# Kernel optimization log

Measured on AMD Instinct MI355X. Metric: run time of the kernel, lower is better.

Reference implementation:

```python
import jax, jax.numpy as jnp
import numpy as np
from jax import lax

B, K, Z, C, H, W = 32, 7, 64, 3, 64, 64
G = H + 6  # decoder grid for 'small' variant
ITERS = 3
SCALE = Z ** -0.5
EPS = 1e-8


def _pe(h, w):
    # matches SlotAttention.create_positional_embedding: shape [w, h, 4]
    ww = jnp.linspace(0.0, 1.0, w)
    hh = jnp.linspace(0.0, 1.0, h)
    a = jnp.broadcast_to((1.0 - ww)[:, None], (w, h))  # dist_right
    b = jnp.broadcast_to(ww[:, None], (w, h))          # dist_left
    c = jnp.broadcast_to(hh[None, :], (w, h))          # dist_top
    d = jnp.broadcast_to((1.0 - hh)[None, :], (w, h))  # dist_bottom
    return jnp.stack([a, b, c, d], -1)


def _ln(x, g, b):
    m = x.mean(-1, keepdims=True)
    v = ((x - m) ** 2).mean(-1, keepdims=True)
    return (x - m) * lax.rsqrt(v + 1e-5) * g + b


def _conv(x, w, b, p):
    y = lax.conv_general_dilated(x, w, (1, 1), [(p, p), (p, p)],
                                 dimension_numbers=('NCHW', 'OIHW', 'NCHW'))
    return y + b[None, :, None, None]


def setup_inputs() -> dict:
    key = jax.random.key(0)
    ks = iter(jax.random.split(key, 64))
    nrm = lambda shape, s=0.05: jax.random.normal(next(ks), shape, jnp.float32) * s
    d = {}
    d['inputs'] = jax.random.normal(next(ks), (B, C, H, W), jnp.float32)
    d['noise'] = jax.random.normal(next(ks), (B * K, Z), jnp.float32)
    d['enc_pos_w'] = nrm((4, 64)); d['enc_pos_b'] = jnp.zeros(64, jnp.float32)
    d['ec1_w'] = nrm((64, 3, 5, 5)); d['ec1_b'] = jnp.zeros(64, jnp.float32)
    d['ec2_w'] = nrm((64, 64, 5, 5)); d['ec2_b'] = jnp.zeros(64, jnp.float32)
    d['ec3_w'] = nrm((64, 64, 5, 5)); d['ec3_b'] = jnp.zeros(64, jnp.float32)
    d['ec4_w'] = nrm((64, 64, 5, 5)); d['ec4_b'] = jnp.zeros(64, jnp.float32)
    d['ln1_g'] = jnp.ones(64, jnp.float32); d['ln1_b'] = jnp.zeros(64, jnp.float32)
    d['fc1_w'] = nrm((64, 64)); d['fc1_b'] = jnp.zeros(64, jnp.float32)
    d['fc2_w'] = nrm((64, 64)); d['fc2_b'] = jnp.zeros(64, jnp.float32)
    d['lns_g'] = jnp.ones(Z, jnp.float32); d['lns_b'] = jnp.zeros(Z, jnp.float32)
    d['lnf_g'] = jnp.ones(Z, jnp.float32); d['lnf_b'] = jnp.zeros(Z, jnp.float32)
    d['q_w'] = nrm((Z, Z)); d['k_w'] = nrm((64, Z)); d['v_w'] = nrm((64, Z))
    d['mlp1_w'] = nrm((Z, 128)); d['mlp1_b'] = jnp.zeros(128, jnp.float32)
    d['mlp2_w'] = nrm((128, Z)); d['mlp2_b'] = jnp.zeros(Z, jnp.float32)
    d['gru_wih'] = nrm((3 * Z, Z)); d['gru_whh'] = nrm((3 * Z, Z))
    d['gru_bih'] = jnp.zeros(3 * Z, jnp.float32); d['gru_bhh'] = jnp.zeros(3 * Z, jnp.float32)
    d['init_slots'] = jnp.concatenate([jnp.zeros((1, Z), jnp.float32), jnp.ones((1, Z), jnp.float32)], 1)
    d['dec_pos_w'] = nrm((4, Z)); d['dec_pos_b'] = jnp.zeros(Z, jnp.float32)
    d['dc1_w'] = nrm((32, Z, 5, 5)); d['dc1_b'] = jnp.zeros(32, jnp.float32)
    d['dc2_w'] = nrm((32, 32, 5, 5)); d['dc2_b'] = jnp.zeros(32, jnp.float32)
    d['dc3_w'] = nrm((32, 32, 5, 5)); d['dc3_b'] = jnp.zeros(32, jnp.float32)
    d['dc4_w'] = nrm((4, 32, 3, 3)); d['dc4_b'] = jnp.zeros(4, jnp.float32)
    return d


def _forward(inputs, noise, enc_pos_w, enc_pos_b, ec1_w, ec1_b, ec2_w, ec2_b,
             ec3_w, ec3_b, ec4_w, ec4_b, ln1_g, ln1_b, fc1_w, fc1_b, fc2_w, fc2_b,
             lns_g, lns_b, lnf_g, lnf_b, q_w, k_w, v_w, mlp1_w, mlp1_b, mlp2_w,
             mlp2_b, gru_wih, gru_whh, gru_bih, gru_bhh, init_slots, dec_pos_w,
             dec_pos_b, dc1_w, dc1_b, dc2_w, dc2_b, dc3_w, dc3_b, dc4_w, dc4_b):
    # ---- encoder ----
    h = jax.nn.relu(_conv(inputs, ec1_w, ec1_b, 2))
    h = jax.nn.relu(_conv(h, ec2_w, ec2_b, 2))
    h = jax.nn.relu(_conv(h, ec3_w, ec3_b, 2))
    h = jax.nn.relu(_conv(h, ec4_w, ec4_b, 2))
    h = h.transpose(0, 2, 3, 1)                        # [B,H,W,64]
    pe = _pe(H, W) @ enc_pos_w + enc_pos_b             # [W,H,64] (H==W)
    h = h + pe[None]
    feat = h.reshape(B, H * W, 64)
    feat = _ln(feat, ln1_g, ln1_b)
    feat = jax.nn.relu(feat @ fc1_w + fc1_b) @ fc2_w + fc2_b
    k = feat @ k_w                                     # [B,N,Z]
    v = feat @ v_w
    # ---- slot init: Normal(loc, softplus(sp)).rsample() ----
    loc, sp = jnp.split(init_slots, 2, axis=1)
    slots = (loc + jax.nn.softplus(sp) * noise).reshape(B, K, Z)
    # ---- iterative slot attention ----
    for _ in range(ITERS):
        prev = slots
        q = (_ln(prev, lns_g, lns_b) @ q_w) * SCALE
        dots = jnp.einsum('bid,bjd->bij', q, k)        # [B,K,N]
        attn = jax.nn.softmax(dots, axis=1) + EPS      # normalize over slots
        attn = attn / attn.sum(-1, keepdims=True)      # renormalize over keys
        updates = jnp.einsum('bjd,bij->bid', v, attn)  # [B,K,Z]
        # GRU cell (single step), torch gate order r,z,n
        gi = updates.reshape(-1, Z) @ gru_wih.T + gru_bih
        gh = prev.reshape(-1, Z) @ gru_whh.T + gru_bhh
        ir, iz, inn = jnp.split(gi, 3, -1)
        hr, hz, hn = jnp.split(gh, 3, -1)
        r = jax.nn.sigmoid(ir + hr)
        zg = jax.nn.sigmoid(iz + hz)
        n = jnp.tanh(inn + r * hn)
        slots = ((1.0 - zg) * n + zg * prev.reshape(-1, Z)).reshape(B, K, Z)
        slots = slots + (jax.nn.relu(_ln(slots, lnf_g, lnf_b) @ mlp1_w + mlp1_b) @ mlp2_w + mlp2_b)
    # ---- spatial-broadcast decoder ('small') ----
    flat = slots.reshape(B * K, Z)
    zb = jnp.broadcast_to(flat[:, :, None, None], (B * K, Z, G, G))
    pe_d = (_pe(G, G) @ dec_pos_w + dec_pos_b).transpose(2, 0, 1)  # [Z,G,G]
    zb = zb + pe_d[None]
    o = jax.nn.relu(_conv(zb, dc1_w, dc1_b, 1))        # 70->68
    o = jax.nn.relu(_conv(o, dc2_w, dc2_b, 1))         # 68->66
    o = jax.nn.relu(_conv(o, dc3_w, dc3_b, 1))         # 66->64
    o = _conv(o, dc4_w, dc4_b, 1)                      # 64->64, 4ch
    x_loc = jax.nn.sigmoid(o[:, :3]).reshape(B, K, C, H, W)
    mask_logits = o[:, 3].reshape(B, K, 1, H, W)
    mask_logp = jax.nn.log_softmax(mask_logits, axis=1)
    x_orig = (inputs + 1.0) / 2.0
    recon = (x_loc * jnp.exp(mask_logp)).sum(1)
    mse = ((x_orig - recon) ** 2).sum() / B
    return mse, x_loc, mask_logp, slots


def reference(inputs, noise, enc_pos_w, enc_pos_b, ec1_w, ec1_b, ec2_w, ec2_b,
              ec3_w, ec3_b, ec4_w, ec4_b, ln1_g, ln1_b, fc1_w, fc1_b, fc2_w, fc2_b,
              lns_g, lns_b, lnf_g, lnf_b, q_w, k_w, v_w, mlp1_w, mlp1_b, mlp2_w,
              mlp2_b, gru_wih, gru_whh, gru_bih, gru_bhh, init_slots, dec_pos_w,
              dec_pos_b, dc1_w, dc1_b, dc2_w, dc2_b, dc3_w, dc3_b, dc4_w, dc4_b):
    return _forward(inputs, noise, enc_pos_w, enc_pos_b, ec1_w, ec1_b, ec2_w, ec2_b,
                    ec3_w, ec3_b, ec4_w, ec4_b, ln1_g, ln1_b, fc1_w, fc1_b, fc2_w, fc2_b,
                    lns_g, lns_b, lnf_g, lnf_b, q_w, k_w, v_w, mlp1_w, mlp1_b, mlp2_w,
                    mlp2_b, gru_wih, gru_whh, gru_bih, gru_bhh, init_slots, dec_pos_w,
                    dec_pos_b, dc1_w, dc1_b, dc2_w, dc2_b, dc3_w, dc3_b, dc4_w, dc4_b)
```

## Files before the change

kernel.cpp:

```cpp
#include <hip/hip_runtime.h>
#include <math.h>

typedef short bf16x8 __attribute__((ext_vector_type(8)));
typedef float f32x4 __attribute__((ext_vector_type(4)));

#define WS_B0   0u
#define WS_B1   4194304u
#define WS_K    8388608u
#define WS_V    16777216u
#define WS_ATTN 25165824u
#define WS_PART 26083328u
#define WS_SLOT 26327040u
#define WS_ROW  26341376u
#define SCALE_ 0.125f

#define OFF_PEB   0u
#define OFF_WCLS  160000u
#define OFF_S     180000u
#define OFF_ZB    250000u

__device__ __forceinline__ float wave_sum(float v) {
#pragma unroll
    for (int m = 32; m >= 1; m >>= 1) v += __shfl_xor(v, m, 64);
    return v;
}
__device__ __forceinline__ unsigned short f2bf(float f) {
    unsigned u = __float_as_uint(f);
    u = u + 0x7fffu + ((u >> 16) & 1u);
    return (unsigned short)(u >> 16);
}
__device__ __forceinline__ float bf2f(unsigned short h) {
    return __uint_as_float(((unsigned)h) << 16);
}

__global__ __launch_bounds__(256) void pack_weights(
    const float* __restrict__ w, unsigned short* __restrict__ wp,
    int CIN, int COUT_STORE, int KS, int NT, int total)
{
    int t = blockIdx.x * 256 + threadIdx.x;
    if (t >= total) return;
    int lane = t & 63;
    int nt = (t >> 6) % NT;
    int ch = t / (64 * NT);
    int CPT = CIN / 32;
    int cic = ch % CPT;
    int tap = ch / CPT;
    int ky = tap / KS, kx = tap % KS;
    int co = nt * 16 + (lane & 15);
    int k0 = cic * 32 + (lane >> 4) * 8;
    unsigned short v[8];
#pragma unroll
    for (int j = 0; j < 8; ++j) {
        int ci = k0 + j;
        float f = (co < COUT_STORE) ? w[((size_t)(co * CIN + ci) * KS + ky) * KS + kx] : 0.f;
        v[j] = f2bf(f);
    }
    *(uint4*)(wp + (size_t)t * 8) = *(uint4*)v;
}

__global__ __launch_bounds__(256) void pack_fc(
    const float* __restrict__ w, unsigned short* __restrict__ wp)
{
    int t = blockIdx.x * 256 + threadIdx.x;
    if (t >= 512) return;
    int lane = t & 63;
    int nt = (t >> 6) & 3;
    int ck = t >> 8;
    int n = nt * 16 + (lane & 15);
    int k0 = ck * 32 + (lane >> 4) * 8;
    unsigned short v[8];
#pragma unroll
    for (int j = 0; j < 8; ++j) v[j] = f2bf(w[(size_t)(k0 + j) * 64 + n]);
    *(uint4*)(wp + (size_t)t * 8) = *(uint4*)v;
}

template<int CIN, int COUT, int KS, int PAD, int NSTORE, int RELU, int OUTF32>
__global__ __launch_bounds__(256) void conv_mfma(
    const unsigned short* __restrict__ in, const unsigned short* __restrict__ wpack,
    const float* __restrict__ bias, void* __restrict__ outv,
    int Hin, int Win, int Hout, int Wout, int tilesX, int tilesY)
{
    constexpr int TS = 16, TH = TS + KS - 1;
    constexpr int NT = COUT / 16;
    constexpr int CPT = CIN / 32;
    constexpr int G8 = CIN / 8;
    __shared__ __align__(16) unsigned short tile[TH][TH][CIN];
    const int tpb = tilesX * tilesY;
    const int n = blockIdx.x / tpb;
    const int t = blockIdx.x % tpb;
    const int ty0 = (t / tilesX) * TS, tx0 = (t % tilesX) * TS;
    const int tid = threadIdx.x;

    const unsigned short* inb = in + (size_t)n * Hin * Win * CIN;
    for (int idx = tid; idx < TH * TH * G8; idx += 256) {
        int g = idx % G8;
        int c = (idx / G8) % TH;
        int r = idx / (G8 * TH);
        int iy = ty0 - PAD + r, ix = tx0 - PAD + c;
        uint4 vv = make_uint4(0, 0, 0, 0);
        if (iy >= 0 && iy < Hin && ix >= 0 && ix < Win)
            vv = *(const uint4*)(inb + ((size_t)iy * Win + ix) * CIN + g * 8);
        int slot = (g * 8 + c * 8) % CIN;
        *(uint4*)&tile[r][c][slot] = vv;
    }
    __syncthreads();

    const int wv = tid >> 6, lane = tid & 63;
    const int q = lane >> 4, m = lane & 15;
    f32x4 acc[4][NT];
#pragma unroll
    for (int mt = 0; mt < 4; ++mt)
#pragma unroll
        for (int nt = 0; nt < NT; ++nt) acc[mt][nt] = (f32x4){0.f, 0.f, 0.f, 0.f};

    for (int tap = 0; tap < KS * KS; ++tap) {
        const int ky = tap / KS, kx = tap % KS;
        const int cbase = m + kx;
#pragma unroll
        for (int cic = 0; cic < CPT; ++cic) {
            const int ch = tap * CPT + cic;
            bf16x8 bfr[NT];
#pragma unroll
            for (int nt = 0; nt < NT; ++nt)
                bfr[nt] = *(const bf16x8*)(wpack + ((size_t)(ch * NT + nt) * 64 + lane) * 8);
            const int slot = (cic * 32 + q * 8 + cbase * 8) % CIN;
#pragma unroll
            for (int mt = 0; mt < 4; ++mt) {
                const int orow = wv * 4 + mt;
                bf16x8 afr = *(const bf16x8*)&tile[orow + ky][cbase][slot];
#pragma unroll
                for (int nt = 0; nt < NT; ++nt)
                    acc[mt][nt] = __builtin_amdgcn_mfma_f32_16x16x32_bf16(afr, bfr[nt], acc[mt][nt], 0, 0, 0);
            }
        }
    }

#pragma unroll
    for (int nt = 0; nt < NT; ++nt) {
        const int co = nt * 16 + m;
        const float bv = (co < NSTORE) ? bias[co] : 0.f;
#pragma unroll
        for (int mt = 0; mt < 4; ++mt) {
            const int oy = ty0 + wv * 4 + mt;
#pragma unroll
            for (int j = 0; j < 4; ++j) {
                const int ox = tx0 + q * 4 + j;
                if (oy < Hout && ox < Wout && co < NSTORE) {
                    float v = acc[mt][nt][j] + bv;
                    if (RELU) v = fmaxf(v, 0.f);
                    size_t o = (((size_t)n * Hout + oy) * Wout + ox) * NSTORE + co;
                    if (OUTF32) ((float*)outv)[o] = v;
                    else ((unsigned short*)outv)[o] = f2bf(v);
                }
            }
        }
    }
}

__global__ __launch_bounds__(256) void pe_synth(
    const float* __restrict__ dpw, const float* __restrict__ dpb,
    unsigned short* __restrict__ peb, float* __restrict__ zbias)
{
    const int tid = threadIdx.x;
    if (blockIdx.x == 0 && tid < 32) zbias[tid] = 0.f;
    const int pix = blockIdx.x * 256 + tid;
    if (pix >= 4900) return;
    const int iy = pix / 70, ix = pix % 70;
    const float fy = iy * (1.f / 69.f), fx = ix * (1.f / 69.f);
    unsigned short v[64];
#pragma unroll
    for (int ci = 0; ci < 64; ++ci) {
        float p = (1.f - fy) * dpw[ci] + fy * dpw[64 + ci]
                + fx * dpw[128 + ci] + (1.f - fx) * dpw[192 + ci] + dpb[ci];
        v[ci] = f2bf(p);
    }
    uint4* ob = (uint4*)(peb + (size_t)pix * 64);
#pragma unroll
    for (int i = 0; i < 8; ++i) ob[i] = ((uint4*)v)[i];
}

__global__ __launch_bounds__(256) void wcls_build(
    const float* __restrict__ w, float* __restrict__ wcls)
{
    int idx = blockIdx.x * 256 + threadIdx.x;
    if (idx >= 9 * 32 * 64) return;
    int cls = idx / (32 * 64);
    int co = (idx / 64) % 32;
    int ci = idx % 64;
    int rc = cls / 3, cc = cls % 3;
    int ky0 = (rc == 0) ? 1 : 0, ky1 = (rc == 2) ? 3 : 4;
    int kx0 = (cc == 0) ? 1 : 0, kx1 = (cc == 2) ? 3 : 4;
    float s = 0.f;
    const float* wb = w + (size_t)(co * 64 + ci) * 25;
    for (int ky = ky0; ky <= ky1; ++ky)
        for (int kx = kx0; kx <= kx1; ++kx)
            s += wb[ky * 5 + kx];
    wcls[idx] = s;
}

__global__ __launch_bounds__(256) void slot_s(
    const float* __restrict__ slots, const float* __restrict__ wcls,
    float* __restrict__ S)
{
    int idx = blockIdx.x * 256 + threadIdx.x;
    if (idx >= 224 * 9 * 32) return;
    int n = idx / (9 * 32);
    int cls = (idx / 32) % 9;
    int co = idx % 32;
    const float* sl = slots + n * 64;
    const float* wc = wcls + (size_t)(cls * 32 + co) * 64;
    float s = 0.f;
#pragma unroll
    for (int ci = 0; ci < 64; ++ci) s = fmaf(sl[ci], wc[ci], s);
    S[idx] = s;
}

__global__ __launch_bounds__(256) void dc1_assemble(
    const float* __restrict__ P,
    const float* __restrict__ S,
    const float* __restrict__ bias,
    int n0,
    unsigned short* __restrict__ out)
{
    const int gid = blockIdx.x * 256 + threadIdx.x;
    const int nl = gid / 4624;
    const int pix = gid % 4624;
    const int oy = pix / 68, ox = pix % 68;
    const int rc = (oy == 0) ? 0 : ((oy == 67) ? 2 : 1);
    const int cc = (ox == 0) ? 0 : ((ox == 67) ? 2 : 1);
    const float* Sp = S + ((size_t)(n0 + nl) * 9 + (rc * 3 + cc)) * 32;
    const float* Pp = P + (size_t)pix * 32;
    unsigned short v[32];
#pragma unroll
    for (int co = 0; co < 32; ++co)
        v[co] = f2bf(fmaxf(bias[co] + Pp[co] + Sp[co], 0.f));
    uint4* ob = (uint4*)(out + ((size_t)nl * 4624 + pix) * 32);
#pragma unroll
    for (int i = 0; i < 4; ++i) ob[i] = ((uint4*)v)[i];
}

__global__ __launch_bounds__(256) void conv_ec1(
    const float* __restrict__ in, const float* __restrict__ wts,
    const float* __restrict__ bias, unsigned short* __restrict__ out)
{
    __shared__ float tile[3][20][21];
    const int blk = blockIdx.x;
    const int n = blk >> 6;
    const int sub = blk & 63;
    const int t = sub >> 2;
    const int cog = sub & 3;
    const int ty0 = (t >> 2) * 16, tx0 = (t & 3) * 16;
    const int tid = threadIdx.x;
    for (int idx = tid; idx < 1200; idx += 256) {
        int ci = idx / 400, rc = idx % 400;
        int r = rc / 20, c = rc % 20;
        int gy = ty0 + r - 2, gx = tx0 + c - 2;
        float v = 0.f;
        if (gy >= 0 && gy < 64 && gx >= 0 && gx < 64)
            v = in[((size_t)n * 3 + ci) * 4096 + gy * 64 + gx];
        tile[ci][r][c] = v;
    }
    __syncthreads();
    const int lx = tid & 15, ly = tid >> 4;
    float acc[16];
#pragma unroll
    for (int co = 0; co < 16; ++co) acc[co] = bias[cog * 16 + co];
    for (int ci = 0; ci < 3; ++ci) {
        float val[25];
#pragma unroll
        for (int ky = 0; ky < 5; ++ky)
#pragma unroll
            for (int kx = 0; kx < 5; ++kx) val[ky * 5 + kx] = tile[ci][ly + ky][lx + kx];
#pragma unroll
        for (int co = 0; co < 16; ++co) {
            const float* wc = wts + (size_t)((cog * 16 + co) * 3 + ci) * 25;
            float a = acc[co];
#pragma unroll
            for (int tt = 0; tt < 25; ++tt) a = fmaf(val[tt], wc[tt], a);
            acc[co] = a;
        }
    }
    unsigned short tmp[16];
#pragma unroll
    for (int co = 0; co < 16; ++co) tmp[co] = f2bf(fmaxf(acc[co], 0.f));
    uint4* ob = (uint4*)(out + (((size_t)n * 64 + ty0 + ly) * 64 + tx0 + lx) * 64 + cog * 16);
    ob[0] = ((uint4*)tmp)[0];
    ob[1] = ((uint4*)tmp)[1];
}

__global__ __launch_bounds__(256) void encoder_tail_mfma(
    const unsigned short* __restrict__ h4,
    const float* __restrict__ epw, const float* __restrict__ epb,
    const float* __restrict__ ln1g, const float* __restrict__ ln1b,
    const unsigned short* __restrict__ pfc1, const float* __restrict__ fc1b,
    const unsigned short* __restrict__ pfc2, const float* __restrict__ fc2b,
    const unsigned short* __restrict__ pkw, const unsigned short* __restrict__ pvw,
    float* __restrict__ kout, float* __restrict__ vout)
{
    __shared__ __align__(16) unsigned short X[64][72];
    const int b = blockIdx.x >> 6;
    const int y = blockIdx.x & 63;
    const int tid = threadIdx.x;

    {
        const int p = tid >> 2, sub = tid & 3;
        const unsigned short* hp = h4 + ((((size_t)b * 64 + y) * 64 + p) * 64) + sub * 16;
        unsigned short raw[16];
        *(uint4*)(raw)     = *(const uint4*)hp;
        *(uint4*)(raw + 8) = *(const uint4*)(hp + 8);
        const float fy = y * (1.f / 63.f), fx = p * (1.f / 63.f);
        float f[16];
        float s1 = 0.f, s2 = 0.f;
#pragma unroll
        for (int j = 0; j < 16; ++j) {
            int ch = sub * 16 + j;
            float pe = (1.f - fy) * epw[ch] + fy * epw[64 + ch]
                     + fx * epw[128 + ch] + (1.f - fx) * epw[192 + ch] + epb[ch];
            float v = bf2f(raw[j]) + pe;
            f[j] = v;
            s1 += v;
            s2 += v * v;
        }
        s1 += __shfl_xor(s1, 1, 64); s1 += __shfl_xor(s1, 2, 64);
        s2 += __shfl_xor(s2, 1, 64); s2 += __shfl_xor(s2, 2, 64);
        const float m = s1 * (1.f / 64.f);
        const float var = s2 * (1.f / 64.f) - m * m;
        const float inv = rsqrtf(var + 1e-5f);
        unsigned short xb[16];
#pragma unroll
        for (int j = 0; j < 16; ++j) {
            int ch = sub * 16 + j;
            xb[j] = f2bf((f[j] - m) * inv * ln1g[ch] + ln1b[ch]);
        }
        *(uint4*)&X[p][sub * 16]     = ((uint4*)xb)[0];
        *(uint4*)&X[p][sub * 16 + 8] = ((uint4*)xb)[1];
    }
    __syncthreads();

    const int w = tid >> 6, lane = tid & 63;
    const int q = lane >> 4, m_ = lane & 15;
    const int row0 = w * 16;

    {
        f32x4 a1[4];
#pragma unroll
        for (int nt = 0; nt < 4; ++nt) a1[nt] = (f32x4){0.f, 0.f, 0.f, 0.f};
#pragma unroll
        for (int ck = 0; ck < 2; ++ck) {
            bf16x8 afr = *(const bf16x8*)&X[row0 + m_][ck * 32 + q * 8];
#pragma unroll
            for (int nt = 0; nt < 4; ++nt) {
                bf16x8 bfr = *(const bf16x8*)(pfc1 + ((size_t)((ck * 4 + nt) * 64 + lane)) * 8);
                a1[nt] = __builtin_amdgcn_mfma_f32_16x16x32_bf16(afr, bfr, a1[nt], 0, 0, 0);
            }
        }
        __syncthreads();
#pragma unroll
        for (int nt = 0; nt < 4; ++nt) {
            const float bb = fc1b[nt * 16 + m_];
#pragma unroll
            for (int reg = 0; reg < 4; ++reg)
                X[row0 + q * 4 + reg][nt * 16 + m_] = f2bf(fmaxf(a1[nt][reg] + bb, 0.f));
        }
    }
    __syncthreads();

    {
        f32x4 a2[4];
#pragma unroll
        for (int nt = 0; nt < 4; ++nt) a2[nt] = (f32x4){0.f, 0.f, 0.f, 0.f};
#pragma unroll
        for (int ck = 0; ck < 2; ++ck) {
            bf16x8 afr = *(const bf16x8*)&X[row0 + m_][ck * 32 + q * 8];
#pragma unroll
            for (int nt = 0; nt < 4; ++nt) {
                bf16x8 bfr = *(const bf16x8*)(pfc2 + ((size_t)((ck * 4 + nt) * 64 + lane)) * 8);
                a2[nt] = __builtin_amdgcn_mfma_f32_16x16x32_bf16(afr, bfr, a2[nt], 0, 0, 0);
            }
        }
        __syncthreads();
#pragma unroll
        for (int nt = 0; nt < 4; ++nt) {
            const float bb = fc2b[nt * 16 + m_];
#pragma unroll
            for (int reg = 0; reg < 4; ++reg)
                X[row0 + q * 4 + reg][nt * 16 + m_] = f2bf(a2[nt][reg] + bb);
        }
    }
    __syncthreads();

    {
        f32x4 ak[4], av[4];
#pragma unroll
        for (int nt = 0; nt < 4; ++nt) {
            ak[nt] = (f32x4){0.f, 0.f, 0.f, 0.f};
            av[nt] = (f32x4){0.f, 0.f, 0.f, 0.f};
        }
#pragma unroll
        for (int ck = 0; ck < 2; ++ck) {
            bf16x8 afr = *(const bf16x8*)&X[row0 + m_][ck * 32 + q * 8];
#pragma unroll
            for (int nt = 0; nt < 4; ++nt) {
                bf16x8 bk = *(const bf16x8*)(pkw + ((size_t)((ck * 4 + nt) * 64 + lane)) * 8);
                bf16x8 bv = *(const bf16x8*)(pvw + ((size_t)((ck * 4 + nt) * 64 + lane)) * 8);
                ak[nt] = __builtin_amdgcn_mfma_f32_16x16x32_bf16(afr, bk, ak[nt], 0, 0, 0);
                av[nt] = __builtin_amdgcn_mfma_f32_16x16x32_bf16(afr, bv, av[nt], 0, 0, 0);
            }
        }
        const size_t base = ((size_t)b * 4096) + y * 64 + row0;
#pragma unroll
        for (int nt = 0; nt < 4; ++nt) {
            const int ch = nt * 16 + m_;
#pragma unroll
            for (int reg = 0; reg < 4; ++reg) {
                const size_t o = (base + q * 4 + reg) * 64 + ch;
                kout[o] = ak[nt][reg];
                vout[o] = av[nt][reg];
            }
        }
    }
}

__global__ __launch_bounds__(256) void slot_init(
    const float* __restrict__ noise, const float* __restrict__ init_slots,
    float* __restrict__ slots, float* __restrict__ rowsum)
{
    int i = blockIdx.x * 256 + threadIdx.x;
    if (i < 224) rowsum[i] = 0.f;
    if (i < 224 * 64) {
        int z = i & 63;
        float spl = log1pf(expf(init_slots[64 + z]));
        slots[i] = init_slots[z] + spl * noise[i];
    }
}

__global__ __launch_bounds__(256) void attn_pass1(
    const float* __restrict__ kbuf, const float* __restrict__ slots,
    const float* __restrict__ lnsg, const float* __restrict__ lnsb,
    const float* __restrict__ qw,
    float* __restrict__ attn, float* __restrict__ rowsum)
{
    __shared__ float qs[7][64];
    __shared__ float red[7][4];
    const int b = blockIdx.x >> 4;
    const int jb = (blockIdx.x & 15) * 256;
    const int tid = threadIdx.x;
    const int lane = tid & 63, wv = tid >> 6;
    for (int i = wv; i < 7; i += 4) {
        float s = slots[(b * 7 + i) * 64 + lane];
        float m = wave_sum(s) * (1.f / 64.f);
        float d = s - m;
        float var = wave_sum(d * d) * (1.f / 64.f);
        float x = d * rsqrtf(var + 1e-5f) * lnsg[lane] + lnsb[lane];
        float qv = 0.f;
        for (int c = 0; c < 64; ++c) qv = fmaf(__shfl(x, c, 64), qw[c * 64 + lane], qv);
        qs[i][lane] = qv * SCALE_;
    }
    __syncthreads();
    const int j = jb + tid;
    float kr[64];
    const float* kp = kbuf + (((size_t)b * 4096) + j) * 64;
#pragma unroll
    for (int d4 = 0; d4 < 16; ++d4) {
        float4 kv = ((const float4*)kp)[d4];
        kr[d4 * 4 + 0] = kv.x; kr[d4 * 4 + 1] = kv.y;
        kr[d4 * 4 + 2] = kv.z; kr[d4 * 4 + 3] = kv.w;
    }
    float dots[7];
#pragma unroll
    for (int i = 0; i < 7; ++i) {
        float a = 0.f;
#pragma unroll
        for (int d = 0; d < 64; ++d) a = fmaf(kr[d], qs[i][d], a);
        dots[i] = a;
    }
    float mx = dots[0];
#pragma unroll
    for (int i = 1; i < 7; ++i) mx = fmaxf(mx, dots[i]);
    float sum = 0.f;
#pragma unroll
    for (int i = 0; i < 7; ++i) { dots[i] = expf(dots[i] - mx); sum += dots[i]; }
    const float inv = 1.f / sum;
#pragma unroll
    for (int i = 0; i < 7; ++i) {
        float a = dots[i] * inv + 1e-8f;
        dots[i] = a;
        attn[(((size_t)b * 7) + i) * 4096 + j] = a;
    }
#pragma unroll
    for (int i = 0; i < 7; ++i) {
        float s = wave_sum(dots[i]);
        if (lane == 0) red[i][wv] = s;
    }
    __syncthreads();
    if (tid < 7) {
        float s = red[tid][0] + red[tid][1] + red[tid][2] + red[tid][3];
        atomicAdd(&rowsum[b * 7 + tid], s);
    }
}

__global__ __launch_bounds__(256) void attn_pass2(
    const float* __restrict__ vbuf, const float* __restrict__ attn,
    float* __restrict__ part)
{
    const int b = blockIdx.x >> 4;
    const int js = blockIdx.x & 15;
    const int tid = threadIdx.x;
    const int d = tid & 63, jc = tid >> 6;
    float acc[7];
#pragma unroll
    for (int i = 0; i < 7; ++i) acc[i] = 0.f;
    const int j0 = js * 256;
    for (int j = j0 + jc; j < j0 + 256; j += 4) {
        float av = vbuf[(((size_t)b * 4096) + j) * 64 + d];
#pragma unroll
        for (int i = 0; i < 7; ++i)
            acc[i] = fmaf(attn[(((size_t)b * 7) + i) * 4096 + j], av, acc[i]);
    }
    __shared__ float red[4][7][64];
#pragma unroll
    for (int i = 0; i < 7; ++i) red[jc][i][d] = acc[i];
    __syncthreads();
    if (tid < 7 * 64) {
        int i = tid / 64, dd = tid % 64;
        float s = red[0][i][dd] + red[1][i][dd] + red[2][i][dd] + red[3][i][dd];
        part[((((size_t)b * 16) + js) * 7 + i) * 64 + dd] = s;
    }
}

__global__ __launch_bounds__(64) void gru_mlp(
    float* __restrict__ slots, const float* __restrict__ part,
    float* __restrict__ rowsum,
    const float* __restrict__ wih, const float* __restrict__ whh,
    const float* __restrict__ bih, const float* __restrict__ bhh,
    const float* __restrict__ lnfg, const float* __restrict__ lnfb,
    const float* __restrict__ m1w, const float* __restrict__ m1b,
    const float* __restrict__ m2w, const float* __restrict__ m2b)
{
    const int n = blockIdx.x;
    const int b = n / 7, i = n % 7;
    const int l = threadIdx.x;
    float upd = 0.f;
    for (int js = 0; js < 16; ++js)
        upd += part[((((size_t)b * 16) + js) * 7 + i) * 64 + l];
    upd /= rowsum[n];
    if (l == 0) rowsum[n] = 0.f;
    const float prev = slots[n * 64 + l];
    float gi0 = bih[l], gi1 = bih[64 + l], gi2 = bih[128 + l];
    float gh0 = bhh[l], gh1 = bhh[64 + l], gh2 = bhh[128 + l];
    for (int c = 0; c < 64; ++c) {
        float u = __shfl(upd, c, 64), p = __shfl(prev, c, 64);
        gi0 = fmaf(u, wih[l * 64 + c], gi0);
        gi1 = fmaf(u, wih[(64 + l) * 64 + c], gi1);
        gi2 = fmaf(u, wih[(128 + l) * 64 + c], gi2);
        gh0 = fmaf(p, whh[l * 64 + c], gh0);
        gh1 = fmaf(p, whh[(64 + l) * 64 + c], gh1);
        gh2 = fmaf(p, whh[(128 + l) * 64 + c], gh2);
    }
    float r  = 1.f / (1.f + expf(-(gi0 + gh0)));
    float zg = 1.f / (1.f + expf(-(gi1 + gh1)));
    float nn = tanhf(gi2 + r * gh2);
    float s = (1.f - zg) * nn + zg * prev;
    float m = wave_sum(s) * (1.f / 64.f);
    float d = s - m;
    float var = wave_sum(d * d) * (1.f / 64.f);
    float x = d * rsqrtf(var + 1e-5f) * lnfg[l] + lnfb[l];
    float h0 = m1b[l], h1 = m1b[64 + l];
    for (int c = 0; c < 64; ++c) {
        float xv = __shfl(x, c, 64);
        h0 = fmaf(xv, m1w[c * 128 + l], h0);
        h1 = fmaf(xv, m1w[c * 128 + 64 + l], h1);
    }
    h0 = fmaxf(h0, 0.f); h1 = fmaxf(h1, 0.f);
    float o = m2b[l];
    for (int c = 0; c < 64; ++c) {
        o = fmaf(__shfl(h0, c, 64), m2w[c * 64 + l], o);
        o = fmaf(__shfl(h1, c, 64), m2w[(64 + c) * 64 + l], o);
    }
    slots[n * 64 + l] = s + o;
}

__global__ __launch_bounds__(256) void finalize_k(
    const float* __restrict__ dc4out, const float* __restrict__ inputs,
    float* __restrict__ out)
{
    const int tid = threadIdx.x;
    const int gp = blockIdx.x * 256 + tid;
    const int b = gp >> 12, p = gp & 4095;
    float4 o4[7];
#pragma unroll
    for (int k = 0; k < 7; ++k)
        o4[k] = ((const float4*)dc4out)[(size_t)(b * 7 + k) * 4096 + p];
    float mx = o4[0].w;
#pragma unroll
    for (int k = 1; k < 7; ++k) mx = fmaxf(mx, o4[k].w);
    float s = 0.f;
#pragma unroll
    for (int k = 0; k < 7; ++k) s += expf(o4[k].w - mx);
    const float lse = mx + logf(s);
    float recon0 = 0.f, recon1 = 0.f, recon2 = 0.f;
    float* xl = out + 1;
    float* ml = out + 2752513;
#pragma unroll
    for (int k = 0; k < 7; ++k) {
        float lp = o4[k].w - lse;
        ml[((size_t)(b * 7 + k)) * 4096 + p] = lp;
        float w = expf(lp);
        float x0 = 1.f / (1.f + expf(-o4[k].x));
        float x1 = 1.f / (1.f + expf(-o4[k].y));
        float x2 = 1.f / (1.f + expf(-o4[k].z));
        xl[(((size_t)(b * 7 + k)) * 3 + 0) * 4096 + p] = x0;
        xl[(((size_t)(b * 7 + k)) * 3 + 1) * 4096 + p] = x1;
        xl[(((size_t)(b * 7 + k)) * 3 + 2) * 4096 + p] = x2;
        recon0 = fmaf(x0, w, recon0);
        recon1 = fmaf(x1, w, recon1);
        recon2 = fmaf(x2, w, recon2);
    }
    float err = 0.f;
    {
        float xo = (inputs[((size_t)b * 3 + 0) * 4096 + p] + 1.f) * 0.5f;
        float dd = xo - recon0; err += dd * dd;
        xo = (inputs[((size_t)b * 3 + 1) * 4096 + p] + 1.f) * 0.5f;
        dd = xo - recon1; err += dd * dd;
        xo = (inputs[((size_t)b * 3 + 2) * 4096 + p] + 1.f) * 0.5f;
        dd = xo - recon2; err += dd * dd;
    }
    float wsum = wave_sum(err);
    __shared__ float red[4];
    const int lane = tid & 63, wv = tid >> 6;
    if (lane == 0) red[wv] = wsum;
    __syncthreads();
    if (tid == 0) atomicAdd(out, (red[0] + red[1] + red[2] + red[3]) * (1.f / 32.f));
}

__global__ __launch_bounds__(256) void copy_slots(const float* __restrict__ slots,
                                                  float* __restrict__ out)
{
    int i = blockIdx.x * 256 + threadIdx.x;
    if (i == 0) out[0] = 0.f;
    if (i < 14336) out[3670017 + i] = slots[i];
}

extern "C" void kernel_launch(void* const* d_in, const int* in_sizes, int n_in,
                              void* d_out, int out_size, void* d_ws, size_t ws_size,
                              hipStream_t stream) {
    (void)in_sizes; (void)n_in; (void)out_size; (void)ws_size;
    const float* inputs = (const float*)d_in[0];
    const float* noise  = (const float*)d_in[1];
    const float* epw  = (const float*)d_in[2];
    const float* epb  = (const float*)d_in[3];
    const float* ec1w = (const float*)d_in[4];
    const float* ec1b = (const float*)d_in[5];
    const float* ec2w = (const float*)d_in[6];
    const float* ec2b = (const float*)d_in[7];
    const float* ec3w = (const float*)d_in[8];
    const float* ec3b = (const float*)d_in[9];
    const float* ec4w = (const float*)d_in[10];
    const float* ec4b = (const float*)d_in[11];
    const float* ln1g = (const float*)d_in[12];
    const float* ln1b = (const float*)d_in[13];
    const float* fc1w = (const float*)d_in[14];
    const float* fc1b = (const float*)d_in[15];
    const float* fc2w = (const float*)d_in[16];
    const float* fc2b = (const float*)d_in[17];
    const float* lnsg = (const float*)d_in[18];
    const float* lnsb = (const float*)d_in[19];
    const float* lnfg = (const float*)d_in[20];
    const float* lnfb = (const float*)d_in[21];
    const float* qw   = (const float*)d_in[22];
    const float* kw   = (const float*)d_in[23];
    const float* vw   = (const float*)d_in[24];
    const float* m1w  = (const float*)d_in[25];
    const float* m1b  = (const float*)d_in[26];
    const float* m2w  = (const float*)d_in[27];
    const float* m2b  = (const float*)d_in[28];
    const float* wih  = (const float*)d_in[29];
    const float* whh  = (const float*)d_in[30];
    const float* bih  = (const float*)d_in[31];
    const float* bhh  = (const float*)d_in[32];
    const float* init_slots = (const float*)d_in[33];
    const float* dpw  = (const float*)d_in[34];
    const float* dpb  = (const float*)d_in[35];
    const float* dc1w = (const float*)d_in[36];
    const float* dc1b = (const float*)d_in[37];
    const float* dc2w = (const float*)d_in[38];
    const float* dc2b = (const float*)d_in[39];
    const float* dc3w = (const float*)d_in[40];
    const float* dc3b = (const float*)d_in[41];
    const float* dc4w = (const float*)d_in[42];
    const float* dc4b = (const float*)d_in[43];

    float* ws = (float*)d_ws;
    unsigned short* B0 = (unsigned short*)(ws + WS_B0);
    unsigned short* B1 = (unsigned short*)(ws + WS_B1);
    float* K = ws + WS_K;
    float* V = ws + WS_V;
    unsigned short* dping = (unsigned short*)(ws + WS_B0);
    unsigned short* dpong = (unsigned short*)(ws + WS_K);
    float* dc4out = V;
    unsigned short* PK = (unsigned short*)(ws + WS_V + 4194304u);
    unsigned short* p_ec2 = PK, *p_ec3 = PK + 102400, *p_ec4 = PK + 204800;
    unsigned short* p_dc1 = PK, *p_dc2 = PK + 51200, *p_dc3 = PK + 76800, *p_dc4 = PK + 102400;
    float* attn  = ws + WS_ATTN;
    unsigned short* PFC = (unsigned short*)attn;
    unsigned short* p_fc1 = PFC, *p_fc2 = PFC + 4096, *p_kw = PFC + 8192, *p_vw = PFC + 12288;
    unsigned short* peb = (unsigned short*)(attn + OFF_PEB);
    float* wclsb = attn + OFF_WCLS;
    float* Sbuf  = attn + OFF_S;
    float* zbias = attn + OFF_ZB;
    float* part  = ws + WS_PART;
    float* P     = ws + WS_PART;
    float* slots = ws + WS_SLOT;
    float* rowsum = ws + WS_ROW;
    float* out = (float*)d_out;

    pack_weights<<<50, 256, 0, stream>>>(ec2w, p_ec2, 64, 64, 5, 4, 12800);
    pack_weights<<<50, 256, 0, stream>>>(ec3w, p_ec3, 64, 64, 5, 4, 12800);
    pack_weights<<<50, 256, 0, stream>>>(ec4w, p_ec4, 64, 64, 5, 4, 12800);
    pack_fc<<<2, 256, 0, stream>>>(fc1w, p_fc1);
    pack_fc<<<2, 256, 0, stream>>>(fc2w, p_fc2);
    pack_fc<<<2, 256, 0, stream>>>(kw, p_kw);
    pack_fc<<<2, 256, 0, stream>>>(vw, p_vw);

    conv_ec1<<<2048, 256, 0, stream>>>(inputs, ec1w, ec1b, B0);
    conv_mfma<64, 64, 5, 2, 64, 1, 0><<<512, 256, 0, stream>>>(B0, p_ec2, ec2b, B1, 64, 64, 64, 64, 4, 4);
    conv_mfma<64, 64, 5, 2, 64, 1, 0><<<512, 256, 0, stream>>>(B1, p_ec3, ec3b, B0, 64, 64, 64, 64, 4, 4);
    conv_mfma<64, 64, 5, 2, 64, 1, 0><<<512, 256, 0, stream>>>(B0, p_ec4, ec4b, B1, 64, 64, 64, 64, 4, 4);
    encoder_tail_mfma<<<2048, 256, 0, stream>>>(B1, epw, epb, ln1g, ln1b,
                                                p_fc1, fc1b, p_fc2, fc2b, p_kw, p_vw, K, V);
    slot_init<<<56, 256, 0, stream>>>(noise, init_slots, slots, rowsum);

    for (int it = 0; it < 3; ++it) {
        attn_pass1<<<512, 256, 0, stream>>>(K, slots, lnsg, lnsb, qw, attn, rowsum);
        attn_pass2<<<512, 256, 0, stream>>>(V, attn, part);
        gru_mlp<<<224, 64, 0, stream>>>(slots, part, rowsum, wih, whh, bih, bhh,
                                        lnfg, lnfb, m1w, m1b, m2w, m2b);
    }

    pack_weights<<<25, 256, 0, stream>>>(dc1w, p_dc1, 64, 32, 5, 2, 6400);
    pack_weights<<<13, 256, 0, stream>>>(dc2w, p_dc2, 32, 32, 5, 2, 3200);
    pack_weights<<<13, 256, 0, stream>>>(dc3w, p_dc3, 32, 32, 5, 2, 3200);
    pack_weights<<<3, 256, 0, stream>>>(dc4w, p_dc4, 32, 4, 3, 1, 576);
    pe_synth<<<20, 256, 0, stream>>>(dpw, dpb, peb, zbias);
    conv_mfma<64, 32, 5, 1, 32, 0, 1><<<25, 256, 0, stream>>>(peb, p_dc1, zbias, P, 70, 70, 68, 68, 5, 5);
    wcls_build<<<72, 256, 0, stream>>>(dc1w, wclsb);
    slot_s<<<252, 256, 0, stream>>>(slots, wclsb, Sbuf);

    for (int ch = 0; ch < 2; ++ch) {
        float* d4o = dc4out + (size_t)ch * 112 * 4 * 4096;
        dc1_assemble<<<2023, 256, 0, stream>>>(P, Sbuf, dc1b, ch * 112, dping);
        conv_mfma<32, 32, 5, 1, 32, 1, 0><<<2800, 256, 0, stream>>>(dping, p_dc2, dc2b, dpong, 68, 68, 66, 66, 5, 5);
        conv_mfma<32, 32, 5, 1, 32, 1, 0><<<1792, 256, 0, stream>>>(dpong, p_dc3, dc3b, dping, 66, 66, 64, 64, 4, 4);
        conv_mfma<32, 16, 3, 1, 4, 0, 1><<<1792, 256, 0, stream>>>(dping, p_dc4, dc4b, d4o, 64, 64, 64, 64, 4, 4);
    }

    copy_slots<<<56, 256, 0, stream>>>(slots, out);
    finalize_k<<<512, 256, 0, stream>>>(dc4out, inputs, out);
}
```

Measured before the change: 841.0 us.

## Reorder conv MFMA loop for A-fragment reuse across ky; store K/V as bf16

The implicit-GEMM conv kernel now iterates over input channel chunk and kx, preloads the B fragments for every ky, and loads each tile row once, reusing it across all ky taps that touch it. This cuts LDS reads of the A fragment from 4*KS per (cic,kx) to KS+3, at the cost of holding KS*NT B fragments in registers, which may raise VGPR pressure. Separately, the K and V projections are written as bf16 instead of fp32 and converted back on load in the attention passes. This halves their memory traffic but reduces attention precision.

```diff
diff --git a/kernel.cpp b/kernel.cpp
--- a/kernel.cpp
+++ b/kernel.cpp
@@ -107,30 +107,37 @@
 
     const int wv = tid >> 6, lane = tid & 63;
     const int q = lane >> 4, m = lane & 15;
+    const int row0 = wv * 4;
     f32x4 acc[4][NT];
 #pragma unroll
     for (int mt = 0; mt < 4; ++mt)
 #pragma unroll
         for (int nt = 0; nt < NT; ++nt) acc[mt][nt] = (f32x4){0.f, 0.f, 0.f, 0.f};
 
-    for (int tap = 0; tap < KS * KS; ++tap) {
-        const int ky = tap / KS, kx = tap % KS;
-        const int cbase = m + kx;
-#pragma unroll
-        for (int cic = 0; cic < CPT; ++cic) {
-            const int ch = tap * CPT + cic;
-            bf16x8 bfr[NT];
-#pragma unroll
-            for (int nt = 0; nt < NT; ++nt)
-                bfr[nt] = *(const bf16x8*)(wpack + ((size_t)(ch * NT + nt) * 64 + lane) * 8);
+#pragma unroll
+    for (int cic = 0; cic < CPT; ++cic) {
+#pragma unroll
+        for (int kx = 0; kx < KS; ++kx) {
+            bf16x8 B[KS][NT];
+#pragma unroll
+            for (int ky = 0; ky < KS; ++ky)
+#pragma unroll
+                for (int nt = 0; nt < NT; ++nt)
+                    B[ky][nt] = *(const bf16x8*)(wpack +
+                        ((size_t)(((ky * KS + kx) * CPT + cic) * NT + nt) * 64 + lane) * 8);
+            const int cbase = m + kx;
             const int slot = (cic * 32 + q * 8 + cbase * 8) % CIN;
 #pragma unroll
-            for (int mt = 0; mt < 4; ++mt) {
-                const int orow = wv * 4 + mt;
-                bf16x8 afr = *(const bf16x8*)&tile[orow + ky][cbase][slot];
-#pragma unroll
-                for (int nt = 0; nt < NT; ++nt)
-                    acc[mt][nt] = __builtin_amdgcn_mfma_f32_16x16x32_bf16(afr, bfr[nt], acc[mt][nt], 0, 0, 0);
+            for (int ir = 0; ir < KS + 3; ++ir) {
+                bf16x8 afr = *(const bf16x8*)&tile[row0 + ir][cbase][slot];
+#pragma unroll
+                for (int ky = 0; ky < KS; ++ky) {
+                    const int mt = ir - ky;
+                    if (mt < 0 || mt > 3) continue;
+#pragma unroll
+                    for (int nt = 0; nt < NT; ++nt)
+                        acc[mt][nt] = __builtin_amdgcn_mfma_f32_16x16x32_bf16(afr, B[ky][nt], acc[mt][nt], 0, 0, 0);
+                }
             }
         }
     }
@@ -216,10 +223,8 @@
 }
 
 __global__ __launch_bounds__(256) void dc1_assemble(
-    const float* __restrict__ P,
-    const float* __restrict__ S,
-    const float* __restrict__ bias,
-    int n0,
+    const float* __restrict__ P, const float* __restrict__ S,
+    const float* __restrict__ bias, int n0,
     unsigned short* __restrict__ out)
 {
     const int gid = blockIdx.x * 256 + threadIdx.x;
@@ -295,7 +300,7 @@
     const unsigned short* __restrict__ pfc1, const float* __restrict__ fc1b,
     const unsigned short* __restrict__ pfc2, const float* __restrict__ fc2b,
     const unsigned short* __restrict__ pkw, const unsigned short* __restrict__ pvw,
-    float* __restrict__ kout, float* __restrict__ vout)
+    unsigned short* __restrict__ kout, unsigned short* __restrict__ vout)
 {
     __shared__ __align__(16) unsigned short X[64][72];
     const int b = blockIdx.x >> 6;
@@ -414,8 +419,8 @@
 #pragma unroll
             for (int reg = 0; reg < 4; ++reg) {
                 const size_t o = (base + q * 4 + reg) * 64 + ch;
-                kout[o] = ak[nt][reg];
-                vout[o] = av[nt][reg];
+                kout[o] = f2bf(ak[nt][reg]);
+                vout[o] = f2bf(av[nt][reg]);
             }
         }
     }
@@ -435,7 +440,7 @@
 }
 
 __global__ __launch_bounds__(256) void attn_pass1(
-    const float* __restrict__ kbuf, const float* __restrict__ slots,
+    const unsigned short* __restrict__ kbuf, const float* __restrict__ slots,
     const float* __restrict__ lnsg, const float* __restrict__ lnsb,
     const float* __restrict__ qw,
     float* __restrict__ attn, float* __restrict__ rowsum)
@@ -459,12 +464,13 @@
     __syncthreads();
     const int j = jb + tid;
     float kr[64];
-    const float* kp = kbuf + (((size_t)b * 4096) + j) * 64;
-#pragma unroll
-    for (int d4 = 0; d4 < 16; ++d4) {
-        float4 kv = ((const float4*)kp)[d4];
-        kr[d4 * 4 + 0] = kv.x; kr[d4 * 4 + 1] = kv.y;
-        kr[d4 * 4 + 2] = kv.z; kr[d4 * 4 + 3] = kv.w;
+    const unsigned short* kp = kbuf + (((size_t)b * 4096) + j) * 64;
+#pragma unroll
+    for (int d8 = 0; d8 < 8; ++d8) {
+        uint4 kv = ((const uint4*)kp)[d8];
+        const unsigned short* h = (const unsigned short*)&kv;
+#pragma unroll
+        for (int z = 0; z < 8; ++z) kr[d8 * 8 + z] = bf2f(h[z]);
     }
     float dots[7];
 #pragma unroll
@@ -500,7 +506,7 @@
 }
 
 __global__ __launch_bounds__(256) void attn_pass2(
-    const float* __restrict__ vbuf, const float* __restrict__ attn,
+    const unsigned short* __restrict__ vbuf, const float* __restrict__ attn,
     float* __restrict__ part)
 {
     const int b = blockIdx.x >> 4;
@@ -512,7 +518,7 @@
     for (int i = 0; i < 7; ++i) acc[i] = 0.f;
     const int j0 = js * 256;
     for (int j = j0 + jc; j < j0 + 256; j += 4) {
-        float av = vbuf[(((size_t)b * 4096) + j) * 64 + d];
+        float av = bf2f(vbuf[(((size_t)b * 4096) + j) * 64 + d]);
 #pragma unroll
         for (int i = 0; i < 7; ++i)
             acc[i] = fmaf(attn[(((size_t)b * 7) + i) * 4096 + j], av, acc[i]);
@@ -693,11 +699,11 @@
     float* ws = (float*)d_ws;
     unsigned short* B0 = (unsigned short*)(ws + WS_B0);
     unsigned short* B1 = (unsigned short*)(ws + WS_B1);
-    float* K = ws + WS_K;
-    float* V = ws + WS_V;
+    unsigned short* K = (unsigned short*)(ws + WS_K);
+    unsigned short* V = (unsigned short*)(ws + WS_V);
     unsigned short* dping = (unsigned short*)(ws + WS_B0);
     unsigned short* dpong = (unsigned short*)(ws + WS_K);
-    float* dc4out = V;
+    float* dc4out = ws + WS_V;
     unsigned short* PK = (unsigned short*)(ws + WS_V + 4194304u);
     unsigned short* p_ec2 = PK, *p_ec3 = PK + 102400, *p_ec4 = PK + 204800;
     unsigned short* p_dc1 = PK, *p_dc2 = PK + 51200, *p_dc3 = PK + 76800, *p_dc4 = PK + 102400;
```

Result: faster. 763.3 us (-9.2%).
